# Optimization experiments

Hardware: AMD Instinct MI355X
Metric: run time of the kernel (lower is better)

The kernel has to match this reference:

```python
import jax, jax.numpy as jnp
import numpy as np

B, T, D, H = 2, 2048, 1024, 16
HD = D // H  # head_dim = 64


def setup_inputs() -> dict:
    key = jax.random.key(0)
    ks = jax.random.split(key, 6)
    std = 1.0 / np.sqrt(D)
    return {
        "x": jax.random.normal(ks[0], (B, T, D), dtype=jnp.float32),
        "q": jax.random.normal(ks[1], (B, T, D), dtype=jnp.float32),
        "kv_w": jax.random.normal(ks[2], (D, 2 * D), dtype=jnp.float32) * std,
        "kv_b": jnp.zeros((2 * D,), dtype=jnp.float32),
        "out_w": jax.random.normal(ks[3], (D, D), dtype=jnp.float32) * std,
        "out_b": jnp.zeros((D,), dtype=jnp.float32),
    }


def reference(x, q, kv_w, kv_b, out_w, out_b):
    b, t_kv, c = x.shape
    t_q = q.shape[1]
    scale = np.sqrt(HD).astype(np.float32)
    # kv projection -> k, v: [B, H, T_kv, HD]
    kv = x @ kv_w + kv_b  # [B, T_kv, 2D]
    k, v = jnp.split(kv, 2, axis=-1)
    k = k.reshape(b, t_kv, H, HD).transpose(0, 2, 1, 3)
    v = v.reshape(b, t_kv, H, HD).transpose(0, 2, 1, 3)
    qh = q.reshape(b, t_q, H, HD).transpose(0, 2, 1, 3)  # [B, H, T_q, HD]
    # non-fused attention: materialize full score matrix [B, H, T_q, T_kv]
    scores = jnp.einsum("bhqd,bhkd->bhqk", qh, k) / scale
    probs = jax.nn.softmax(scores, axis=-1)
    attn = jnp.einsum("bhqk,bhkd->bhqd", probs, v)  # [B, H, T_q, HD]
    attn = attn.transpose(0, 2, 1, 3).reshape(b, t_q, c)
    return attn @ out_w + out_b
```

## Files before the change

### kernel.cpp

```cpp
#include <hip/hip_runtime.h>
#include <hip/hip_bf16.h>

typedef __bf16 bf16_t;
typedef __attribute__((ext_vector_type(8))) __bf16 bf16x8;
typedef __attribute__((ext_vector_type(4))) float f32x4;
typedef __attribute__((ext_vector_type(2))) unsigned int u32x2;
typedef unsigned int u32;
typedef unsigned short u16;


__device__ __forceinline__ u32 pack2(float a, float b) {
    u16 ua = __builtin_bit_cast(u16, (bf16_t)a);
    u16 ub = __builtin_bit_cast(u16, (bf16_t)b);
    return (u32)ua | ((u32)ub << 16);
}

__device__ __forceinline__ bf16x8 cvt8(float4 f0, float4 f1) {
    bf16x8 v;
    v[0]=(bf16_t)f0.x; v[1]=(bf16_t)f0.y; v[2]=(bf16_t)f0.z; v[3]=(bf16_t)f0.w;
    v[4]=(bf16_t)f1.x; v[5]=(bf16_t)f1.y; v[6]=(bf16_t)f1.z; v[7]=(bf16_t)f1.w;
    return v;
}

__device__ __forceinline__ float exp2_fast(float x) {
    float r;
    asm("v_exp_f32 %0, %1" : "=v"(r) : "v"(x));
    return r;
}

__device__ __forceinline__ void gload_lds16(const void* g, void* l) {
    __builtin_amdgcn_global_load_lds(
        (const __attribute__((address_space(1))) unsigned int*)g,
        (__attribute__((address_space(3))) unsigned int*)l, 16, 0, 0);
}

__global__ __launch_bounds__(256) void prep_kernel(
    const float* __restrict__ x,
    const float* __restrict__ kv_w,
    const float* __restrict__ out_w,
    bf16_t* __restrict__ xb,
    bf16_t* __restrict__ kv_wt,
    bf16_t* __restrict__ out_wt)
{
    __shared__ bf16_t T[64 * 72];
    const int blk = blockIdx.x;
    const int tid = threadIdx.x;

    if (blk < 1024) {
        const size_t base = (size_t)blk * 4096 + tid * 16;
        const float4* p = (const float4*)(x + base);
        float4 f0 = p[0], f1 = p[1], f2 = p[2], f3 = p[3];
        *(bf16x8*)(xb + base)     = cvt8(f0, f1);
        *(bf16x8*)(xb + base + 8) = cvt8(f2, f3);
        return;
    }

    const bool is_kv = (blk < 1536);
    const int t = is_kv ? (blk - 1024) : (blk - 1536);
    const int k0 = is_kv ? (t >> 5) * 64 : (t >> 4) * 64;
    const int n0 = is_kv ? (t & 31) * 64 : (t & 15) * 64;
    const int srcld = is_kv ? 2048 : 1024;
    const float* W = is_kv ? kv_w : out_w;
    bf16_t* Wt = is_kv ? kv_wt : out_wt;

    {
        const int r = tid >> 2, c4 = (tid & 3) * 16;
        const float4* p = (const float4*)(W + (size_t)(k0 + r) * srcld + n0 + c4);
        float4 f0 = p[0], f1 = p[1], f2 = p[2], f3 = p[3];
        *(bf16x8*)&T[r * 72 + c4]     = cvt8(f0, f1);
        *(bf16x8*)&T[r * 72 + c4 + 8] = cvt8(f2, f3);
    }
    __syncthreads();
    {
        const int n = tid >> 2, kc = (tid & 3) * 16;
        bf16x8 o0, o1;
#pragma unroll
        for (int kk = 0; kk < 8; kk++) o0[kk] = T[(kc + kk) * 72 + n];
#pragma unroll
        for (int kk = 0; kk < 8; kk++) o1[kk] = T[(kc + 8 + kk) * 72 + n];
        *(bf16x8*)(Wt + (size_t)(n0 + n) * 1024 + k0 + kc)     = o0;
        *(bf16x8*)(Wt + (size_t)(n0 + n) * 1024 + k0 + kc + 8) = o1;
    }
}

__global__ __launch_bounds__(256, 2) void kv_gemm_kernel(
    const bf16_t* __restrict__ xb,
    const bf16_t* __restrict__ wt,
    const float* __restrict__ kv_b,
    bf16_t* __restrict__ Kbuf,
    bf16_t* __restrict__ Vt)
{
    __shared__ bf16_t L[2][2][128 * 64];

    const int tid = threadIdx.x;
    const int w = tid >> 6, ln = tid & 63;
    const int g = ln >> 4, qc = ln & 15;
    const int braw = blockIdx.x;
    const int bsw = (braw & 7) * 64 + (braw >> 3);
    const int n0 = (bsw & 15) * 128, m0 = (bsw >> 4) * 128;
    const int wm = (w >> 1) * 64, wn = (w & 1) * 64;
    const int srow = ln >> 3, sslot = ln & 7;
    const int scol = (sslot ^ srow) * 8;

    f32x4 acc[4][4];
    const f32x4 z = {0.f, 0.f, 0.f, 0.f};
#pragma unroll
    for (int i = 0; i < 4; i++)
#pragma unroll
        for (int j = 0; j < 4; j++) acc[i][j] = z;

    const bf16_t* Abase = xb + (size_t)(m0 + w * 32 + srow) * 1024 + scol;
    const bf16_t* Bbase = wt + (size_t)(n0 + w * 32 + srow) * 1024 + scol;

#define KV_STAGE(buf, k0)                                                        \
    {                                                                            \
        _Pragma("unroll")                                                        \
        for (int i = 0; i < 4; i++) {                                            \
            gload_lds16(Abase + (size_t)i * 8 * 1024 + (k0), &L[buf][0][(w * 32 + i * 8) * 64]); \
            gload_lds16(Bbase + (size_t)i * 8 * 1024 + (k0), &L[buf][1][(w * 32 + i * 8) * 64]); \
        }                                                                        \
    }

    KV_STAGE(0, 0);
    __syncthreads();

    int cur = 0;
    const int swz = qc & 7;
    for (int ks = 0; ks < 16; ks++) {
        if (ks < 15) KV_STAGE(cur ^ 1, (ks + 1) * 64);
        bf16x8 af[2][4], bfv[2][4];
#pragma unroll
        for (int kk = 0; kk < 2; kk++) {
#pragma unroll
            for (int i = 0; i < 4; i++)
                af[kk][i]  = *(const bf16x8*)&L[cur][0][(wm + i * 16 + qc) * 64 + (((kk * 4 + g) ^ swz) * 8)];
#pragma unroll
            for (int j = 0; j < 4; j++)
                bfv[kk][j] = *(const bf16x8*)&L[cur][1][(wn + j * 16 + qc) * 64 + (((kk * 4 + g) ^ swz) * 8)];
        }
#pragma unroll
        for (int kk = 0; kk < 2; kk++)
#pragma unroll
            for (int i = 0; i < 4; i++)
#pragma unroll
                for (int j = 0; j < 4; j++)
                    acc[i][j] = __builtin_amdgcn_mfma_f32_16x16x32_bf16(af[kk][i], bfv[kk][j], acc[i][j], 0, 0, 0);
        __syncthreads();
        cur ^= 1;
    }
#undef KV_STAGE

    if (n0 < 1024) {
#pragma unroll
        for (int i = 0; i < 4; i++) {
#pragma unroll
            for (int j = 0; j < 4; j++) {
                const int colg = n0 + wn + j * 16 + qc;
                const float bias = kv_b[colg];
                const int h = colg >> 6, d = colg & 63;
#pragma unroll
                for (int r = 0; r < 4; r++) {
                    const int rowg = m0 + wm + i * 16 + g * 4 + r;
                    const int b = rowg >> 11, t = rowg & 2047;
                    Kbuf[(((size_t)(b * 16 + h) * 2048 + t) << 6) + d] = (bf16_t)(acc[i][j][r] + bias);
                }
            }
        }
    } else {
        bf16_t* T = (bf16_t*)L;
#pragma unroll
        for (int i = 0; i < 4; i++) {
#pragma unroll
            for (int j = 0; j < 4; j++) {
                const int nloc = wn + j * 16 + qc;
                const float bias = kv_b[n0 + nloc];
                const int mloc = wm + i * 16 + g * 4;
                *(u32*)&T[nloc * 134 + mloc]     = pack2(acc[i][j][0] + bias, acc[i][j][1] + bias);
                *(u32*)&T[nloc * 134 + mloc + 2] = pack2(acc[i][j][2] + bias, acc[i][j][3] + bias);
            }
        }
        __syncthreads();
        const int n = tid >> 1, mh = (tid & 1) * 64;
        const int d = n0 - 1024 + n;
        const int b = m0 >> 11;
        const int t0 = (m0 & 2047) + mh;
        bf16_t* dst = Vt + (((size_t)(b * 16 + (d >> 6)) * 64 + (d & 63)) << 11) + t0;
#pragma unroll
        for (int k = 0; k < 8; k++)
            *(bf16x8*)(dst + k * 8) = *(const bf16x8*)&T[n * 134 + mh + k * 8];
    }
}

__global__ __launch_bounds__(256) void attn_kernel(
    const float* __restrict__ q,
    const bf16_t* __restrict__ Kbuf,
    const bf16_t* __restrict__ Vt,
    bf16_t* __restrict__ attn)
{
    __shared__ bf16_t Klds[2][64 * 64];
    __shared__ bf16_t Vlds[2][64 * 64];
    __shared__ bf16_t Plds[4][2][16 * 72];

    const int tid = threadIdx.x;
    const int wv = tid >> 6;
    const int ln = tid & 63;
    const int g = ln >> 4, qc = ln & 15;

    const int braw = blockIdx.x;
    const int bsw = (braw & 7) * 64 + (braw >> 3);
    const int bh = bsw >> 4;
    const int qb = bsw & 15;
    const int b = bh >> 4, h = bh & 15;
    const int q0 = qb * 128 + wv * 32;

    const float qscale = 0.125f * 1.44269504088896f;
    bf16x8 qf[2][2];
#pragma unroll
    for (int qt = 0; qt < 2; qt++) {
        const float* qp = q + ((size_t)(b * 2048 + q0 + qt * 16 + qc) * 1024) + h * 64 + g * 8;
#pragma unroll
        for (int c = 0; c < 2; c++) {
            float4 f0 = *(const float4*)(qp + c * 32);
            float4 f1 = *(const float4*)(qp + c * 32 + 4);
            f0.x*=qscale; f0.y*=qscale; f0.z*=qscale; f0.w*=qscale;
            f1.x*=qscale; f1.y*=qscale; f1.z*=qscale; f1.w*=qscale;
            qf[qt][c] = cvt8(f0, f1);
        }
    }

    const bf16_t* Kb = Kbuf + (size_t)bh * (2048 * 64);
    const bf16_t* Vb = Vt + (size_t)bh * (64 * 2048);

    float l_part[2] = {0.0f, 0.0f};
    f32x4 acc[2][4];
    const f32x4 z = {0.f, 0.f, 0.f, 0.f};
#pragma unroll
    for (int qt = 0; qt < 2; qt++)
#pragma unroll
        for (int dt = 0; dt < 4; dt++) acc[qt][dt] = z;

    const int srow = ln >> 3;
    const int sc16 = ln & 7;

#pragma unroll
    for (int i = 0; i < 2; i++) {
        const int row = wv * 16 + i * 8 + srow;
        const int slot = sc16 ^ (row & 7);
        gload_lds16(Kb + (size_t)row * 64 + slot * 8,       &Klds[0][(wv * 16 + i * 8) * 64]);
        gload_lds16(Vb + (size_t)row * 2048 + 0 + slot * 8, &Vlds[0][(wv * 16 + i * 8) * 64]);
    }
    __syncthreads();

    int cur = 0;
    for (int t = 0; t < 32; ++t) {
        const int kv0 = t * 64;
        if (t + 1 < 32) {
            const int kvn = kv0 + 64;
#pragma unroll
            for (int i = 0; i < 2; i++) {
                const int row = wv * 16 + i * 8 + srow;
                const int slot = sc16 ^ (row & 7);
                gload_lds16(Kb + (size_t)(kvn + row) * 64 + slot * 8, &Klds[cur ^ 1][(wv * 16 + i * 8) * 64]);
                gload_lds16(Vb + (size_t)row * 2048 + kvn + slot * 8, &Vlds[cur ^ 1][(wv * 16 + i * 8) * 64]);
            }
        }

        const bf16_t* Kl = Klds[cur];
        const bf16_t* Vl = Vlds[cur];

        f32x4 st[4][2];
#pragma unroll
        for (int kt = 0; kt < 4; kt++) {
            bf16x8 k0 = *(const bf16x8*)&Kl[(kt * 16 + qc) * 64 + ((g       ^ (qc & 7)) * 8)];
            bf16x8 k1 = *(const bf16x8*)&Kl[(kt * 16 + qc) * 64 + (((4 + g) ^ (qc & 7)) * 8)];
#pragma unroll
            for (int qt = 0; qt < 2; qt++) {
                f32x4 s = __builtin_amdgcn_mfma_f32_16x16x32_bf16(k0, qf[qt][0], z, 0, 0, 0);
                st[kt][qt] = __builtin_amdgcn_mfma_f32_16x16x32_bf16(k1, qf[qt][1], s, 0, 0, 0);
            }
        }

        bf16x8 vf[4][2];
#pragma unroll
        for (int dt = 0; dt < 4; dt++)
#pragma unroll
            for (int ks = 0; ks < 2; ks++)
                vf[dt][ks] = *(const bf16x8*)&Vl[(dt * 16 + qc) * 64 + (((ks * 4 + g) ^ (qc & 7)) * 8)];

#pragma unroll
        for (int qt = 0; qt < 2; qt++) {
            float p[16];
            float s0 = 0.f, s1 = 0.f;
#pragma unroll
            for (int kt = 0; kt < 4; kt++)
#pragma unroll
                for (int r = 0; r < 4; r++) {
                    float pv = exp2_fast(st[kt][qt][r]);
                    p[kt * 4 + r] = pv;
                    if (r & 1) s1 += pv; else s0 += pv;
                }
            l_part[qt] += s0 + s1;

            bf16_t* Pq = &Plds[wv][qt][0];
#pragma unroll
            for (int kt = 0; kt < 4; kt++) {
                u32x2 wpk;
                wpk[0] = pack2(p[kt * 4 + 0], p[kt * 4 + 1]);
                wpk[1] = pack2(p[kt * 4 + 2], p[kt * 4 + 3]);
                *(u32x2*)&Pq[qc * 72 + kt * 16 + g * 4] = wpk;
            }
        }

#pragma unroll
        for (int qt = 0; qt < 2; qt++) {
            bf16x8 pf0 = *(const bf16x8*)&Plds[wv][qt][qc * 72 + g * 8];
            bf16x8 pf1 = *(const bf16x8*)&Plds[wv][qt][qc * 72 + 32 + g * 8];
#pragma unroll
            for (int dt = 0; dt < 4; dt++) {
                acc[qt][dt] = __builtin_amdgcn_mfma_f32_16x16x32_bf16(pf0, vf[dt][0], acc[qt][dt], 0, 0, 0);
                acc[qt][dt] = __builtin_amdgcn_mfma_f32_16x16x32_bf16(pf1, vf[dt][1], acc[qt][dt], 0, 0, 0);
            }
        }

        __syncthreads();
        cur ^= 1;
    }

#pragma unroll
    for (int qt = 0; qt < 2; qt++) {
        float lsum = l_part[qt];
        lsum += __shfl_xor(lsum, 16);
        lsum += __shfl_xor(lsum, 32);
        float li[4];
#pragma unroll
        for (int r = 0; r < 4; r++) li[r] = 1.0f / __shfl(lsum, g * 4 + r);
#pragma unroll
        for (int dt = 0; dt < 4; dt++)
#pragma unroll
            for (int r = 0; r < 4; r++) {
                const float o = acc[qt][dt][r] * li[r];
                const int trow = q0 + qt * 16 + g * 4 + r;
                attn[((size_t)(b * 2048 + trow)) * 1024 + h * 64 + dt * 16 + qc] = (bf16_t)o;
            }
    }
}

__global__ __launch_bounds__(256, 2) void out_gemm_kernel(
    const bf16_t* __restrict__ attn,
    const bf16_t* __restrict__ wt,
    const float* __restrict__ out_b,
    float* __restrict__ out)
{
    __shared__ bf16_t L[2][2][128 * 64];

    const int tid = threadIdx.x;
    const int w = tid >> 6, ln = tid & 63;
    const int g = ln >> 4, qc = ln & 15;
    const int braw = blockIdx.x;
    const int bsw = (braw & 7) * 32 + (braw >> 3);
    const int n0 = (bsw & 7) * 128, m0 = (bsw >> 3) * 128;
    const int wm = (w >> 1) * 64, wn = (w & 1) * 64;
    const int srow = ln >> 3, sslot = ln & 7;
    const int scol = (sslot ^ srow) * 8;

    f32x4 acc[4][4];
    const f32x4 z = {0.f, 0.f, 0.f, 0.f};
#pragma unroll
    for (int i = 0; i < 4; i++)
#pragma unroll
        for (int j = 0; j < 4; j++) acc[i][j] = z;

    const bf16_t* Abase = attn + (size_t)(m0 + w * 32 + srow) * 1024 + scol;
    const bf16_t* Bbase = wt   + (size_t)(n0 + w * 32 + srow) * 1024 + scol;

#define OG_STAGE(buf, k0)                                                        \
    {                                                                            \
        _Pragma("unroll")                                                        \
        for (int i = 0; i < 4; i++) {                                            \
            gload_lds16(Abase + (size_t)i * 8 * 1024 + (k0), &L[buf][0][(w * 32 + i * 8) * 64]); \
            gload_lds16(Bbase + (size_t)i * 8 * 1024 + (k0), &L[buf][1][(w * 32 + i * 8) * 64]); \
        }                                                                        \
    }

    OG_STAGE(0, 0);
    __syncthreads();

    int cur = 0;
    const int swz = qc & 7;
    for (int ks = 0; ks < 16; ks++) {
        if (ks < 15) OG_STAGE(cur ^ 1, (ks + 1) * 64);
        bf16x8 af[2][4], bfv[2][4];
#pragma unroll
        for (int kk = 0; kk < 2; kk++) {
#pragma unroll
            for (int i = 0; i < 4; i++)
                af[kk][i]  = *(const bf16x8*)&L[cur][0][(wm + i * 16 + qc) * 64 + (((kk * 4 + g) ^ swz) * 8)];
#pragma unroll
            for (int j = 0; j < 4; j++)
                bfv[kk][j] = *(const bf16x8*)&L[cur][1][(wn + j * 16 + qc) * 64 + (((kk * 4 + g) ^ swz) * 8)];
        }
#pragma unroll
        for (int kk = 0; kk < 2; kk++)
#pragma unroll
            for (int i = 0; i < 4; i++)
#pragma unroll
                for (int j = 0; j < 4; j++)
                    acc[i][j] = __builtin_amdgcn_mfma_f32_16x16x32_bf16(af[kk][i], bfv[kk][j], acc[i][j], 0, 0, 0);
        __syncthreads();
        cur ^= 1;
    }
#undef OG_STAGE

#pragma unroll
    for (int i = 0; i < 4; i++) {
#pragma unroll
        for (int j = 0; j < 4; j++) {
            const int colg = n0 + wn + j * 16 + qc;
            const float bias = out_b[colg];
#pragma unroll
            for (int r = 0; r < 4; r++) {
                const int rowg = m0 + wm + i * 16 + g * 4 + r;
                out[(size_t)rowg * 1024 + colg] = acc[i][j][r] + bias;
            }
        }
    }
}

extern "C" void kernel_launch(void* const* d_in, const int* in_sizes, int n_in,
                              void* d_out, int out_size, void* d_ws, size_t ws_size,
                              hipStream_t stream) {
    const float* x     = (const float*)d_in[0];
    const float* q     = (const float*)d_in[1];
    const float* kv_w  = (const float*)d_in[2];
    const float* kv_b  = (const float*)d_in[3];
    const float* out_w = (const float*)d_in[4];
    const float* out_b = (const float*)d_in[5];
    float* out = (float*)d_out;

    bf16_t* xb     = (bf16_t*)d_ws;
    bf16_t* kv_wt  = xb + (size_t)4096 * 1024;
    bf16_t* out_wt = kv_wt + (size_t)2048 * 1024;
    bf16_t* Kbuf   = out_wt + (size_t)1024 * 1024;
    bf16_t* Vt     = Kbuf + (size_t)32 * 2048 * 64;
    bf16_t* attnb  = Vt + (size_t)32 * 2048 * 64;

    prep_kernel<<<dim3(1792), 256, 0, stream>>>(x, kv_w, out_w, xb, kv_wt, out_wt);
    kv_gemm_kernel<<<dim3(512), 256, 0, stream>>>(xb, kv_wt, kv_b, Kbuf, Vt);
    attn_kernel<<<dim3(512), 256, 0, stream>>>(q, Kbuf, Vt, attnb);
    out_gemm_kernel<<<dim3(256), 256, 0, stream>>>(attnb, out_wt, out_b, out);
}
```

Baseline: 107.2 us.

## Split attention KV range across two blocks and merge partial outputs

Each attention block now covers half of the key/value sequence, which doubles the grid to 1024 blocks. Each block writes unnormalized bf16 partial outputs and per-row sums into reused workspace buffers. A new merge kernel adds the two partials and divides by the combined sum. The aim is more parallelism and occupancy across the CUs, at the cost of an extra kernel launch, more memory traffic and bf16 rounding of the unnormalized partials.

```diff
diff --git a/kernel.cpp b/kernel.cpp
--- a/kernel.cpp
+++ b/kernel.cpp
@@ -195,7 +195,9 @@
     const float* __restrict__ q,
     const bf16_t* __restrict__ Kbuf,
     const bf16_t* __restrict__ Vt,
-    bf16_t* __restrict__ attn)
+    bf16_t* __restrict__ part0,
+    bf16_t* __restrict__ part1,
+    float* __restrict__ lbuf)
 {
     __shared__ bf16_t Klds[2][64 * 64];
     __shared__ bf16_t Vlds[2][64 * 64];
@@ -207,9 +209,10 @@
     const int g = ln >> 4, qc = ln & 15;
 
     const int braw = blockIdx.x;
-    const int bsw = (braw & 7) * 64 + (braw >> 3);
-    const int bh = bsw >> 4;
-    const int qb = bsw & 15;
+    const int bsw = (braw & 7) * 128 + (braw >> 3);
+    const int bh = bsw >> 5;
+    const int qb = (bsw >> 1) & 15;
+    const int s  = bsw & 1;
     const int b = bh >> 4, h = bh & 15;
     const int q0 = qb * 128 + wv * 32;
 
@@ -228,8 +231,8 @@
         }
     }
 
-    const bf16_t* Kb = Kbuf + (size_t)bh * (2048 * 64);
-    const bf16_t* Vb = Vt + (size_t)bh * (64 * 2048);
+    const bf16_t* Kb = Kbuf + (size_t)bh * (2048 * 64) + (size_t)s * (1024 * 64);
+    const bf16_t* Vb = Vt + (size_t)bh * (64 * 2048) + s * 1024;
 
     float l_part[2] = {0.0f, 0.0f};
     f32x4 acc[2][4];
@@ -252,9 +255,9 @@
     __syncthreads();
 
     int cur = 0;
-    for (int t = 0; t < 32; ++t) {
+    for (int t = 0; t < 16; ++t) {
         const int kv0 = t * 64;
-        if (t + 1 < 32) {
+        if (t + 1 < 16) {
             const int kvn = kv0 + 64;
 #pragma unroll
             for (int i = 0; i < 2; i++) {
@@ -275,8 +278,8 @@
             bf16x8 k1 = *(const bf16x8*)&Kl[(kt * 16 + qc) * 64 + (((4 + g) ^ (qc & 7)) * 8)];
 #pragma unroll
             for (int qt = 0; qt < 2; qt++) {
-                f32x4 s = __builtin_amdgcn_mfma_f32_16x16x32_bf16(k0, qf[qt][0], z, 0, 0, 0);
-                st[kt][qt] = __builtin_amdgcn_mfma_f32_16x16x32_bf16(k1, qf[qt][1], s, 0, 0, 0);
+                f32x4 sacc = __builtin_amdgcn_mfma_f32_16x16x32_bf16(k0, qf[qt][0], z, 0, 0, 0);
+                st[kt][qt] = __builtin_amdgcn_mfma_f32_16x16x32_bf16(k1, qf[qt][1], sacc, 0, 0, 0);
             }
         }
 
@@ -326,23 +329,44 @@
         cur ^= 1;
     }
 
+    bf16_t* Obuf = s ? part1 : part0;
+    float* lp = lbuf + (size_t)s * (32 * 2048);
 #pragma unroll
     for (int qt = 0; qt < 2; qt++) {
         float lsum = l_part[qt];
         lsum += __shfl_xor(lsum, 16);
         lsum += __shfl_xor(lsum, 32);
-        float li[4];
-#pragma unroll
-        for (int r = 0; r < 4; r++) li[r] = 1.0f / __shfl(lsum, g * 4 + r);
+        if (g == 0)
+            lp[(b * 16 + h) * 2048 + q0 + qt * 16 + qc] = lsum;
 #pragma unroll
         for (int dt = 0; dt < 4; dt++)
 #pragma unroll
             for (int r = 0; r < 4; r++) {
-                const float o = acc[qt][dt][r] * li[r];
                 const int trow = q0 + qt * 16 + g * 4 + r;
-                attn[((size_t)(b * 2048 + trow)) * 1024 + h * 64 + dt * 16 + qc] = (bf16_t)o;
-            }
-    }
+                Obuf[((size_t)(b * 2048 + trow)) * 1024 + h * 64 + dt * 16 + qc] = (bf16_t)acc[qt][dt][r];
+            }
+    }
+}
+
+__global__ __launch_bounds__(256) void merge_kernel(
+    const bf16_t* __restrict__ p1,
+    const float* __restrict__ lbuf,
+    bf16_t* __restrict__ p0)
+{
+    const size_t f8 = ((size_t)blockIdx.x * 256 + threadIdx.x) * 8;
+    const int row = (int)(f8 >> 10);
+    const int col = (int)(f8 & 1023);
+    const int b = row >> 11, t = row & 2047;
+    const int h = col >> 6;
+    const int li = (b * 16 + h) * 2048 + t;
+    const float rinv = 1.0f / (lbuf[li] + lbuf[32 * 2048 + li]);
+    bf16x8 a = *(const bf16x8*)(p0 + f8);
+    bf16x8 c = *(const bf16x8*)(p1 + f8);
+    bf16x8 o;
+#pragma unroll
+    for (int k = 0; k < 8; k++)
+        o[k] = (bf16_t)(((float)a[k] + (float)c[k]) * rinv);
+    *(bf16x8*)(p0 + f8) = o;
 }
 
 __global__ __launch_bounds__(256, 2) void out_gemm_kernel(
@@ -446,6 +470,7 @@
 
     prep_kernel<<<dim3(1792), 256, 0, stream>>>(x, kv_w, out_w, xb, kv_wt, out_wt);
     kv_gemm_kernel<<<dim3(512), 256, 0, stream>>>(xb, kv_wt, kv_b, Kbuf, Vt);
-    attn_kernel<<<dim3(512), 256, 0, stream>>>(q, Kbuf, Vt, attnb);
+    attn_kernel<<<dim3(1024), 256, 0, stream>>>(q, Kbuf, Vt, attnb, xb, (float*)kv_wt);
+    merge_kernel<<<dim3(2048), 256, 0, stream>>>(xb, (const float*)kv_wt, attnb);
     out_gemm_kernel<<<dim3(256), 256, 0, stream>>>(attnb, out_wt, out_b, out);
 }
```

Result: slower. 115.1 us (+7.4%).
